# Performance work log

Hardware: AMD Instinct MI355X
Metric: run time of the kernel (lower is better)

## Reference

```python
import jax, jax.numpy as jnp
import numpy as np

WINDOW_SIZE = 256
NEG_INF = jnp.finfo(jnp.float32).min


def setup_inputs() -> dict:
    key = jax.random.key(0)
    kq, kk, kv = jax.random.split(key, 3)
    B, H, S, D = 1, 8, 4096, 128
    q = jax.random.normal(kq, (B, H, S, D), dtype=jnp.float32)
    k = jax.random.normal(kk, (B, H, S, D), dtype=jnp.float32)
    v = jax.random.normal(kv, (B, H, S, D), dtype=jnp.float32)
    return {"q": q, "k": k, "v": v}


def _local_mask(seq_len: int) -> jnp.ndarray:
    idx = jnp.arange(seq_len)
    qi = idx[:, None]
    ki = idx[None, :]
    # causal AND within trailing window of WINDOW_SIZE keys
    return (ki <= qi) & (ki >= qi - WINDOW_SIZE + 1)  # [S, S] bool


def reference(q, k, v):
    B, H, S, D = q.shape
    scale = 1.0 / np.sqrt(D).astype(np.float32)
    mask = _local_mask(S)  # [S, S]
    scores = jnp.einsum('bhsd,bhtd->bhst', q, k) * scale  # [B,H,S,S]
    scores = jnp.where(mask[None, None, :, :], scores, NEG_INF)
    attn = jax.nn.softmax(scores.astype(jnp.float32), axis=-1).astype(q.dtype)
    out = jnp.einsum('bhst,bhtd->bhsd', attn, v)
    return out
```

## Files before the change

kernel.cpp:

```cpp
#include <hip/hip_runtime.h>


typedef __bf16 bf16v8 __attribute__((ext_vector_type(8)));
typedef __bf16 bf16x2 __attribute__((ext_vector_type(2)));
typedef float  f32x4  __attribute__((ext_vector_type(4)));

constexpr int QB = 32, DH = 128, WIN = 256;
constexpr int HSUB = 9;
constexpr float SCALE = 0.08838834764831844f;

constexpr int PSTR  = 296;
constexpr int P_BYTES = QB * PSTR * 2;
constexpr int MB_OFF  = P_BYTES;
constexpr int LB_OFF  = MB_OFF + 64 * 4;
constexpr int SMEM_BYTES = LB_OFF + 64 * 4;

union bfu8 { bf16v8 v; bf16x2 p[4]; };

__device__ __forceinline__ void cvt_hilo8(const float4& a, const float4& b,
                                          bf16v8& hi, bf16v8& lo) {
  float x[8] = {a.x, a.y, a.z, a.w, b.x, b.y, b.z, b.w};
  bfu8 H, L;
#pragma unroll
  for (int j = 0; j < 4; ++j) {
    float x0 = x[2 * j], x1 = x[2 * j + 1];
    __bf16 h0 = (__bf16)x0, h1 = (__bf16)x1;
    H.p[j] = bf16x2{h0, h1};
    L.p[j] = bf16x2{(__bf16)(x0 - (float)h0), (__bf16)(x1 - (float)h1)};
  }
  hi = H.v; lo = L.v;
}
__device__ __forceinline__ unsigned short bfbits(float x) {
  union { __bf16 b; unsigned short u; } c; c.b = (__bf16)x; return c.u;
}
#define MFMA(A, B, C) __builtin_amdgcn_mfma_f32_16x16x32_bf16((A), (B), (C), 0, 0, 0)

__global__ __launch_bounds__(256, 4)
void lwa6(const float* __restrict__ qg, const float* __restrict__ kg,
          const float* __restrict__ vg, float* __restrict__ og, int S) {
  __shared__ __align__(16) char smem[SMEM_BYTES];

  const int bid = blockIdx.x;
  const int h   = bid & 7;
  const int q0  = (bid >> 3) * QB;
  const int tid = threadIdx.x;
  const int wv  = tid >> 6;
  const int lane = tid & 63;
  const int lg  = lane >> 4;
  const int lm  = lane & 15;
  const int rg  = wv & 1;
  const int hf  = wv >> 1;
  const int ts0 = HSUB * hf;

  const float* qgb = qg + (size_t)h * S * DH;
  const float* kgb = kg + (size_t)h * S * DH;
  const float* vgb = vg + (size_t)h * S * DH;

  bf16v8 qhi[4], qlo[4];
  {
    const float* qrow = qgb + (size_t)(q0 + 16 * rg + lm) * DH;
#pragma unroll
    for (int kc = 0; kc < 4; ++kc) {
      float4 a = *(const float4*)(qrow + 32 * kc + 8 * lg);
      float4 b = *(const float4*)(qrow + 32 * kc + 8 * lg + 4);
      a.x *= SCALE; a.y *= SCALE; a.z *= SCALE; a.w *= SCALE;
      b.x *= SCALE; b.y *= SCALE; b.z *= SCALE; b.w *= SCALE;
      cvt_hilo8(a, b, qhi[kc], qlo[kc]);
    }
  }

  f32x4 acc[HSUB];
#pragma unroll
  for (int s = 0; s < HSUB; ++s) acc[s] = (f32x4){0.f, 0.f, 0.f, 0.f};

#pragma unroll
  for (int s = 0; s < HSUB; ++s) {
    const int key0 = q0 - WIN + 16 * (ts0 + s);
    if (key0 < 0) continue;
    const float* kr = kgb + (size_t)(key0 + lm) * DH;
    float4 ka[4], kb_[4];
#pragma unroll
    for (int kc = 0; kc < 4; ++kc) {
      ka[kc]  = *(const float4*)(kr + 32 * kc + 8 * lg);
      kb_[kc] = *(const float4*)(kr + 32 * kc + 8 * lg + 4);
    }
    f32x4 c = acc[s];
#pragma unroll
    for (int kc = 0; kc < 4; ++kc) {
      bf16v8 kh, kl;
      cvt_hilo8(ka[kc], kb_[kc], kh, kl);
      c = MFMA(qhi[kc], kh, c);
      c = MFMA(qlo[kc], kh, c);
      c = MFMA(qhi[kc], kl, c);
    }
    acc[s] = c;
  }

  float* mbuf = (float*)(smem + MB_OFF);
  float* lbuf = (float*)(smem + LB_OFF);

  float mrow[4], rl[4];
#pragma unroll
  for (int r = 0; r < 4; ++r) {
    const int qi = q0 + 16 * rg + 4 * lg + r;
    float m = -3.0e38f;
#pragma unroll
    for (int s = 0; s < HSUB; ++s) {
      const int ki = q0 - WIN + 16 * (ts0 + s) + lm;
      const bool ok = (ki >= 0) && (ki <= qi) && (ki > qi - WIN);
      float v = ok ? acc[s][r] : -3.0e38f;
      acc[s][r] = v;
      m = fmaxf(m, v);
    }
#pragma unroll
    for (int msk = 1; msk < 16; msk <<= 1) m = fmaxf(m, __shfl_xor(m, msk));
    mrow[r] = m;
    if (lm == 0) mbuf[hf * 32 + 16 * rg + 4 * lg + r] = m;
  }
  __syncthreads();
#pragma unroll
  for (int r = 0; r < 4; ++r)
    mrow[r] = fmaxf(mrow[r], mbuf[(1 - hf) * 32 + 16 * rg + 4 * lg + r]);

#pragma unroll
  for (int r = 0; r < 4; ++r) {
    float l = 0.f;
#pragma unroll
    for (int s = 0; s < HSUB; ++s) {
      float p = __expf(acc[s][r] - mrow[r]);
      acc[s][r] = p;
      l += p;
    }
#pragma unroll
    for (int msk = 1; msk < 16; msk <<= 1) l += __shfl_xor(l, msk);
    if (lm == 0) lbuf[hf * 32 + 16 * rg + 4 * lg + r] = l;
    rl[r] = l;
    const int row = 16 * rg + 4 * lg + r;
#pragma unroll
    for (int s = 0; s < HSUB; ++s) {
      const int col = 16 * (ts0 + s) + lm;
      *(unsigned short*)(smem + row * (PSTR * 2) + col * 2) = bfbits(acc[s][r]);
    }
  }
  __syncthreads();
#pragma unroll
  for (int r = 0; r < 4; ++r)
    rl[r] = 1.f / (rl[r] + lbuf[(1 - hf) * 32 + 16 * rg + 4 * lg + r]);

  f32x4 o[4];
#pragma unroll
  for (int n = 0; n < 4; ++n) o[n] = (f32x4){0.f, 0.f, 0.f, 0.f};

#pragma unroll
  for (int kc = 0; kc < 9; ++kc) {
    const int keyb = q0 - WIN + 32 * kc;
    if (keyb < 0) continue;
    const bf16v8 pf = *(const bf16v8*)(smem + (16 * rg + lm) * (PSTR * 2) +
                                       (32 * kc + 8 * lg) * 2);
#pragma unroll
    for (int n = 0; n < 4; ++n) {
      const int d = 64 * hf + 16 * n + lm;
      const float* vp = vgb + (size_t)(keyb + 8 * lg) * DH + d;
      float x[8];
#pragma unroll
      for (int j = 0; j < 8; ++j) x[j] = vp[(size_t)j * DH];
      bfu8 V_;
#pragma unroll
      for (int j = 0; j < 4; ++j)
        V_.p[j] = bf16x2{(__bf16)x[2 * j], (__bf16)x[2 * j + 1]};
      o[n] = MFMA(pf, V_.v, o[n]);
    }
  }

  float* ob = og + (size_t)(h * S + q0 + 16 * rg) * DH;
#pragma unroll
  for (int n = 0; n < 4; ++n)
#pragma unroll
    for (int r = 0; r < 4; ++r)
      ob[(4 * lg + r) * DH + 64 * hf + 16 * n + lm] = o[n][r] * rl[r];
}

extern "C" void kernel_launch(void* const* d_in, const int* in_sizes, int n_in,
                              void* d_out, int out_size, void* d_ws, size_t ws_size,
                              hipStream_t stream) {
  const float* q = (const float*)d_in[0];
  const float* k = (const float*)d_in[1];
  const float* v = (const float*)d_in[2];
  float* out = (float*)d_out;
  const int H = 8, D = 128;
  const int S = in_sizes[0] / (H * D);
  const int nblk = (S / QB) * H;
  lwa6<<<dim3(nblk), 256, 0, stream>>>(q, k, v, out, S);
}
```

Measured before the change: 128.9 us.

## Double-buffer K and V global loads in registers to overlap with MFMA

Adds a two-deep register prefetch pipeline for the K tiles in the QK^T loop and for the V tiles in the PV loop, issuing loads two iterations ahead of use. The first V tiles are also loaded before the softmax phase so their latency is hidden behind it. To hold the larger register buffers, launch bounds drop from 4 to 2 blocks per CU. The intent is to hide global load latency, at the cost of higher register pressure and possibly lower occupancy.

After: 131.2 us. About the same (+1.7%).

```diff
diff --git a/kernel.cpp b/kernel.cpp
--- a/kernel.cpp
+++ b/kernel.cpp
@@ -35,8 +35,8 @@
 }
 #define MFMA(A, B, C) __builtin_amdgcn_mfma_f32_16x16x32_bf16((A), (B), (C), 0, 0, 0)
 
-__global__ __launch_bounds__(256, 4)
-void lwa6(const float* __restrict__ qg, const float* __restrict__ kg,
+__global__ __launch_bounds__(256, 2)
+void lwa7(const float* __restrict__ qg, const float* __restrict__ kg,
           const float* __restrict__ vg, float* __restrict__ og, int S) {
   __shared__ __align__(16) char smem[SMEM_BYTES];
 
@@ -73,28 +73,54 @@
 #pragma unroll
   for (int s = 0; s < HSUB; ++s) acc[s] = (f32x4){0.f, 0.f, 0.f, 0.f};
 
+  float4 kbuf[2][8];
+  auto kload = [&](int s) {
+    const int key0 = q0 - WIN + 16 * (ts0 + s);
+    if (key0 < 0) return;
+    const float* kr = kgb + (size_t)(key0 + lm) * DH;
+#pragma unroll
+    for (int kc = 0; kc < 4; ++kc) {
+      kbuf[s & 1][2 * kc]     = *(const float4*)(kr + 32 * kc + 8 * lg);
+      kbuf[s & 1][2 * kc + 1] = *(const float4*)(kr + 32 * kc + 8 * lg + 4);
+    }
+  };
+  kload(0);
+  kload(1);
 #pragma unroll
   for (int s = 0; s < HSUB; ++s) {
-    const int key0 = q0 - WIN + 16 * (ts0 + s);
-    if (key0 < 0) continue;
-    const float* kr = kgb + (size_t)(key0 + lm) * DH;
-    float4 ka[4], kb_[4];
-#pragma unroll
-    for (int kc = 0; kc < 4; ++kc) {
-      ka[kc]  = *(const float4*)(kr + 32 * kc + 8 * lg);
-      kb_[kc] = *(const float4*)(kr + 32 * kc + 8 * lg + 4);
-    }
-    f32x4 c = acc[s];
-#pragma unroll
-    for (int kc = 0; kc < 4; ++kc) {
-      bf16v8 kh, kl;
-      cvt_hilo8(ka[kc], kb_[kc], kh, kl);
-      c = MFMA(qhi[kc], kh, c);
-      c = MFMA(qlo[kc], kh, c);
-      c = MFMA(qhi[kc], kl, c);
-    }
-    acc[s] = c;
-  }
+    const bool live = (q0 - WIN + 16 * (ts0 + s)) >= 0;
+    bf16v8 kh[4], kl[4];
+    if (live) {
+#pragma unroll
+      for (int kc = 0; kc < 4; ++kc)
+        cvt_hilo8(kbuf[s & 1][2 * kc], kbuf[s & 1][2 * kc + 1], kh[kc], kl[kc]);
+    }
+    if (s + 2 < HSUB) kload(s + 2);
+    if (live) {
+      f32x4 c = acc[s];
+#pragma unroll
+      for (int kc = 0; kc < 4; ++kc) {
+        c = MFMA(qhi[kc], kh[kc], c);
+        c = MFMA(qlo[kc], kh[kc], c);
+        c = MFMA(qhi[kc], kl[kc], c);
+      }
+      acc[s] = c;
+    }
+  }
+
+  float vbuf[2][32];
+  auto vload = [&](int kc) {
+    const int keyb = q0 - WIN + 32 * kc;
+    if (keyb < 0) return;
+    const float* vp = vgb + (size_t)(keyb + 8 * lg) * DH + 64 * hf + lm;
+#pragma unroll
+    for (int n = 0; n < 4; ++n)
+#pragma unroll
+      for (int j = 0; j < 8; ++j)
+        vbuf[kc & 1][8 * n + j] = vp[(size_t)j * DH + 16 * n];
+  };
+  vload(0);
+  vload(1);
 
   float* mbuf = (float*)(smem + MB_OFF);
   float* lbuf = (float*)(smem + LB_OFF);
@@ -154,21 +180,25 @@
 #pragma unroll
   for (int kc = 0; kc < 9; ++kc) {
     const int keyb = q0 - WIN + 32 * kc;
-    if (keyb < 0) continue;
-    const bf16v8 pf = *(const bf16v8*)(smem + (16 * rg + lm) * (PSTR * 2) +
-                                       (32 * kc + 8 * lg) * 2);
-#pragma unroll
-    for (int n = 0; n < 4; ++n) {
-      const int d = 64 * hf + 16 * n + lm;
-      const float* vp = vgb + (size_t)(keyb + 8 * lg) * DH + d;
-      float x[8];
-#pragma unroll
-      for (int j = 0; j < 8; ++j) x[j] = vp[(size_t)j * DH];
-      bfu8 V_;
-#pragma unroll
-      for (int j = 0; j < 4; ++j)
-        V_.p[j] = bf16x2{(__bf16)x[2 * j], (__bf16)x[2 * j + 1]};
-      o[n] = MFMA(pf, V_.v, o[n]);
+    const bool live = keyb >= 0;
+    bf16v8 vf[4];
+    if (live) {
+#pragma unroll
+      for (int n = 0; n < 4; ++n) {
+        bfu8 V_;
+#pragma unroll
+        for (int j2 = 0; j2 < 4; ++j2)
+          V_.p[j2] = bf16x2{(__bf16)vbuf[kc & 1][8 * n + 2 * j2],
+                            (__bf16)vbuf[kc & 1][8 * n + 2 * j2 + 1]};
+        vf[n] = V_.v;
+      }
+    }
+    if (kc + 2 < 9) vload(kc + 2);
+    if (live) {
+      const bf16v8 pf = *(const bf16v8*)(smem + (16 * rg + lm) * (PSTR * 2) +
+                                         (32 * kc + 8 * lg) * 2);
+#pragma unroll
+      for (int n = 0; n < 4; ++n) o[n] = MFMA(pf, vf[n], o[n]);
     }
   }
 
@@ -190,5 +220,5 @@
   const int H = 8, D = 128;
   const int S = in_sizes[0] / (H * D);
   const int nblk = (S / QB) * H;
-  lwa6<<<dim3(nblk), 256, 0, stream>>>(q, k, v, out, S);
-}
+  lwa7<<<dim3(nblk), 256, 0, stream>>>(q, k, v, out, S);
+}
```
